# Optimization experiments

Measured on AMD Instinct MI355X. Metric: run time of the kernel, lower is better.

Reference implementation:

```python
import jax, jax.numpy as jnp
import numpy as np

B, S, IN, OUT, E, K = 4, 4096, 1024, 1024, 8, 2
SCALE = 512.0  # alpha / r = 512 / 1
TEMP = 1.0


def setup_inputs() -> dict:
    key = jax.random.key(0)
    k1, k2, k3, k4 = jax.random.split(key, 4)
    return {
        "x": jax.random.normal(k1, (B, S, IN), dtype=jnp.float32),
        "lora_A": jax.random.normal(k2, (E, 1, IN), dtype=jnp.float32) * 0.02,
        "lora_B": jax.random.normal(k3, (E, OUT, 1), dtype=jnp.float32) * 0.02,
        "gate_w": jax.random.normal(k4, (E, IN), dtype=jnp.float32) * 0.02,
        "gate_b": jnp.zeros((E,), dtype=jnp.float32),
    }


def reference(x, lora_A, lora_B, gate_w, gate_b):
    # segment-level gating: mean over seq, softmax over experts
    seg = x.mean(axis=1)                                    # [B, IN]
    logits = (seg @ gate_w.T + gate_b) / TEMP               # [B, E]
    gate_scores = jax.nn.softmax(logits, axis=-1)           # [B, E]
    topk_scores, topk_idx = jax.lax.top_k(gate_scores, K)   # [B, K] (same for all tokens in segment)

    # dense all-expert LoRA compute (eval mode: dropout is identity)
    h = jnp.einsum('bsi,eri->bser', x, lora_A)              # [B, S, E, r]
    expert_outputs = jnp.einsum('bser,eor->bseo', h, lora_B) * SCALE  # [B, S, E, OUT]

    # gather top-k experts per segment (broadcast over seq) and weighted-sum
    sel = jnp.take_along_axis(expert_outputs, topk_idx[:, None, :, None], axis=2)  # [B, S, K, OUT]
    out = jnp.sum(sel * topk_scores[:, None, :, None], axis=2)  # [B, S, OUT]
    return out
```

## Files before the change

kernel.cpp:

```cpp
#include <hip/hip_runtime.h>

#define SCALE_F 512.0f

#define WS_H     0
#define WS_GPART 131072
#define WS_SELC  147456

__global__ __launch_bounds__(256) void k1_h_gate(
    const float* __restrict__ x, const float* __restrict__ lora_A,
    const float* __restrict__ gate_w, float* __restrict__ h,
    float* __restrict__ gpart)
{
    const int tid  = threadIdx.x;
    const int w    = tid >> 6;
    const int lane = tid & 63;
    const int tok0 = blockIdx.x * 8;

    __shared__ float xbuf[8 * 1024];

    float4 W[4][4];
#pragma unroll
    for (int rr = 0; rr < 4; ++rr) {
        const int row = 4 * w + rr;
        const float* rp = (row < 8) ? (lora_A + row * 1024)
                                    : (gate_w + (row - 8) * 1024);
        const float4* rp4 = (const float4*)rp;
#pragma unroll
        for (int j = 0; j < 4; ++j) W[rr][j] = rp4[lane + 64 * j];
    }

    const float4* src = (const float4*)(x + (size_t)tok0 * 1024);
    float4* dst = (float4*)xbuf;
#pragma unroll
    for (int j = 0; j < 8; ++j) dst[tid + 256 * j] = src[tid + 256 * j];
    __syncthreads();

    float gacc0 = 0.f, gacc1 = 0.f, gacc2 = 0.f, gacc3 = 0.f;

#pragma unroll 2
    for (int t = 0; t < 8; ++t) {
        const float4* xr = (const float4*)(xbuf + t * 1024);
        const float4 xv0 = xr[lane];
        const float4 xv1 = xr[lane + 64];
        const float4 xv2 = xr[lane + 128];
        const float4 xv3 = xr[lane + 192];

        float p[4];
#pragma unroll
        for (int rr = 0; rr < 4; ++rr) {
            const float4 a0 = W[rr][0], a1 = W[rr][1];
            const float4 a2 = W[rr][2], a3 = W[rr][3];
            float s;
            s  = xv0.x * a0.x + xv0.y * a0.y + xv0.z * a0.z + xv0.w * a0.w;
            s += xv1.x * a1.x + xv1.y * a1.y + xv1.z * a1.z + xv1.w * a1.w;
            s += xv2.x * a2.x + xv2.y * a2.y + xv2.z * a2.z + xv2.w * a2.w;
            s += xv3.x * a3.x + xv3.y * a3.y + xv3.z * a3.z + xv3.w * a3.w;
            p[rr] = s;
        }
#pragma unroll
        for (int off = 32; off > 0; off >>= 1) {
            p[0] += __shfl_xor(p[0], off);
            p[1] += __shfl_xor(p[1], off);
            p[2] += __shfl_xor(p[2], off);
            p[3] += __shfl_xor(p[3], off);
        }
        const int tok = tok0 + t;
        if (w < 2) {
            if (lane == 0) {
                float4 hv = make_float4(p[0], p[1], p[2], p[3]);
                *(float4*)(h + (size_t)tok * 8 + w * 4) = hv;
            }
        } else {
            gacc0 += p[0]; gacc1 += p[1]; gacc2 += p[2]; gacc3 += p[3];
        }
    }

    if (w >= 2 && lane == 0) {
        float4 gv = make_float4(gacc0, gacc1, gacc2, gacc3);
        *(float4*)(gpart + (size_t)blockIdx.x * 8 + (w - 2) * 4) = gv;
    }
}

__global__ __launch_bounds__(256) void k2_gate(
    const float* __restrict__ gpart, const float* __restrict__ gate_b,
    int* __restrict__ sel, float* __restrict__ coef)
{
    const int tid  = threadIdx.x;
    const int j    = tid & 7;
    const int pair = tid >> 3;
    const int b    = pair >> 3;
    const int e    = pair & 7;

    __shared__ float s_red[32][8];
    __shared__ float s_logit[32];

    float acc = 0.f;
#pragma unroll 8
    for (int k = 0; k < 64; ++k) {
        acc += gpart[(size_t)(b * 512 + j * 64 + k) * 8 + e];
    }
    s_red[pair][j] = acc;
    __syncthreads();

    if (j == 0) {
        float s = 0.f;
#pragma unroll
        for (int q = 0; q < 8; ++q) s += s_red[pair][q];
        s_logit[pair] = s * (1.0f / 4096.0f) + gate_b[e];
    }
    __syncthreads();

    if (tid < 4) {
        float sc[8];
        float m = -1e30f;
#pragma unroll
        for (int q = 0; q < 8; ++q) { sc[q] = s_logit[tid * 8 + q]; m = fmaxf(m, sc[q]); }
        float sum = 0.f;
#pragma unroll
        for (int q = 0; q < 8; ++q) { sc[q] = __expf(sc[q] - m); sum += sc[q]; }
        const float inv = 1.0f / sum;

        int i0 = 0;
#pragma unroll
        for (int q = 1; q < 8; ++q) if (sc[q] > sc[i0]) i0 = q;
        int i1 = (i0 == 0) ? 1 : 0;
#pragma unroll
        for (int q = 0; q < 8; ++q) if (q != i0 && sc[q] > sc[i1]) i1 = q;

        sel[tid * 2]      = i0;
        sel[tid * 2 + 1]  = i1;
        coef[tid * 2]     = SCALE_F * sc[i0] * inv;
        coef[tid * 2 + 1] = SCALE_F * sc[i1] * inv;
    }
}

__global__ __launch_bounds__(256) void k3_combine(
    const float* __restrict__ h, const int* __restrict__ sel,
    const float* __restrict__ coef, const float* __restrict__ lora_B,
    float* __restrict__ out)
{
    const int tid = threadIdx.x;
    const int blk = blockIdx.x;
    const int b   = blk >> 9;

    const int   i0 = sel[b * 2];
    const int   i1 = sel[b * 2 + 1];
    const float c0 = coef[b * 2];
    const float c1 = coef[b * 2 + 1];

    const float4 b0 = ((const float4*)(lora_B + i0 * 1024))[tid];
    const float4 b1 = ((const float4*)(lora_B + i1 * 1024))[tid];
    const float4 v0 = make_float4(c0 * b0.x, c0 * b0.y, c0 * b0.z, c0 * b0.w);
    const float4 v1 = make_float4(c1 * b1.x, c1 * b1.y, c1 * b1.z, c1 * b1.w);

    const int tok0 = blk * 8;
    float4* out4 = (float4*)out;
#pragma unroll
    for (int t = 0; t < 8; ++t) {
        const int tok = tok0 + t;
        const float h0 = h[tok * 8 + i0];
        const float h1 = h[tok * 8 + i1];
        float4 r;
        r.x = h0 * v0.x + h1 * v1.x;
        r.y = h0 * v0.y + h1 * v1.y;
        r.z = h0 * v0.z + h1 * v1.z;
        r.w = h0 * v0.w + h1 * v1.w;
        out4[(size_t)tok * 256 + tid] = r;
    }
}

extern "C" void kernel_launch(void* const* d_in, const int* in_sizes, int n_in,
                              void* d_out, int out_size, void* d_ws, size_t ws_size,
                              hipStream_t stream) {
    const float* x      = (const float*)d_in[0];
    const float* lora_A = (const float*)d_in[1];
    const float* lora_B = (const float*)d_in[2];
    const float* gate_w = (const float*)d_in[3];
    const float* gate_b = (const float*)d_in[4];
    float* out = (float*)d_out;

    float* ws    = (float*)d_ws;
    float* h     = ws + WS_H;
    float* gpart = ws + WS_GPART;
    int*   sel   = (int*)(ws + WS_SELC);
    float* coef  = ws + WS_SELC + 8;

    k1_h_gate<<<2048, 256, 0, stream>>>(x, lora_A, gate_w, h, gpart);
    k2_gate<<<1, 256, 0, stream>>>(gpart, gate_b, sel, coef);
    k3_combine<<<2048, 256, 0, stream>>>(h, sel, coef, lora_B, out);
}
```

Before: 136.8 us.

## Fuse gate softmax/top-k into combine kernel and defer gate shuffle reduction

Drops the single-block gate kernel: every combine block now reduces the 512 per-block gate partials for its batch, then does its own softmax and top-k before writing output. In the first kernel, the gate-row warps accumulate per-lane partials across tokens and do one cross-lane shuffle reduction at the end instead of one per token, and h is staged in shared memory for the combine step. This removes a launch and a serialized tiny kernel, but each of 2048 blocks redundantly reads 16KB of partials plus several syncs.

```diff
diff --git a/kernel.cpp b/kernel.cpp
--- a/kernel.cpp
+++ b/kernel.cpp
@@ -4,9 +4,8 @@
 
 #define WS_H     0
 #define WS_GPART 131072
-#define WS_SELC  147456
-
-__global__ __launch_bounds__(256) void k1_h_gate(
+
+__global__ __launch_bounds__(256) void kA_h_gate(
     const float* __restrict__ x, const float* __restrict__ lora_A,
     const float* __restrict__ gate_w, float* __restrict__ h,
     float* __restrict__ gpart)
@@ -35,7 +34,7 @@
     for (int j = 0; j < 8; ++j) dst[tid + 256 * j] = src[tid + 256 * j];
     __syncthreads();
 
-    float gacc0 = 0.f, gacc1 = 0.f, gacc2 = 0.f, gacc3 = 0.f;
+    float gacc[4] = {0.f, 0.f, 0.f, 0.f};
 
 #pragma unroll 2
     for (int t = 0; t < 8; ++t) {
@@ -57,68 +56,102 @@
             s += xv3.x * a3.x + xv3.y * a3.y + xv3.z * a3.z + xv3.w * a3.w;
             p[rr] = s;
         }
-#pragma unroll
-        for (int off = 32; off > 0; off >>= 1) {
-            p[0] += __shfl_xor(p[0], off);
-            p[1] += __shfl_xor(p[1], off);
-            p[2] += __shfl_xor(p[2], off);
-            p[3] += __shfl_xor(p[3], off);
-        }
-        const int tok = tok0 + t;
+
         if (w < 2) {
+#pragma unroll
+            for (int off = 32; off > 0; off >>= 1) {
+                p[0] += __shfl_xor(p[0], off);
+                p[1] += __shfl_xor(p[1], off);
+                p[2] += __shfl_xor(p[2], off);
+                p[3] += __shfl_xor(p[3], off);
+            }
             if (lane == 0) {
                 float4 hv = make_float4(p[0], p[1], p[2], p[3]);
-                *(float4*)(h + (size_t)tok * 8 + w * 4) = hv;
+                *(float4*)(h + (size_t)(tok0 + t) * 8 + w * 4) = hv;
             }
         } else {
-            gacc0 += p[0]; gacc1 += p[1]; gacc2 += p[2]; gacc3 += p[3];
-        }
-    }
-
-    if (w >= 2 && lane == 0) {
-        float4 gv = make_float4(gacc0, gacc1, gacc2, gacc3);
-        *(float4*)(gpart + (size_t)blockIdx.x * 8 + (w - 2) * 4) = gv;
-    }
-}
-
-__global__ __launch_bounds__(256) void k2_gate(
-    const float* __restrict__ gpart, const float* __restrict__ gate_b,
-    int* __restrict__ sel, float* __restrict__ coef)
+            gacc[0] += p[0]; gacc[1] += p[1]; gacc[2] += p[2]; gacc[3] += p[3];
+        }
+    }
+
+    if (w >= 2) {
+#pragma unroll
+        for (int off = 32; off > 0; off >>= 1) {
+            gacc[0] += __shfl_xor(gacc[0], off);
+            gacc[1] += __shfl_xor(gacc[1], off);
+            gacc[2] += __shfl_xor(gacc[2], off);
+            gacc[3] += __shfl_xor(gacc[3], off);
+        }
+        if (lane == 0) {
+            float4 gv = make_float4(gacc[0], gacc[1], gacc[2], gacc[3]);
+            *(float4*)(gpart + (size_t)blockIdx.x * 8 + (w - 2) * 4) = gv;
+        }
+    }
+}
+
+static __device__ __forceinline__ float4 f4add(float4 a, float4 b) {
+    return make_float4(a.x + b.x, a.y + b.y, a.z + b.z, a.w + b.w);
+}
+
+__global__ __launch_bounds__(256) void kB_gate_combine(
+    const float* __restrict__ h, const float* __restrict__ gpart,
+    const float* __restrict__ gate_b, const float* __restrict__ lora_B,
+    float* __restrict__ out)
 {
     const int tid  = threadIdx.x;
-    const int j    = tid & 7;
-    const int pair = tid >> 3;
-    const int b    = pair >> 3;
-    const int e    = pair & 7;
-
-    __shared__ float s_red[32][8];
-    __shared__ float s_logit[32];
-
-    float acc = 0.f;
-#pragma unroll 8
-    for (int k = 0; k < 64; ++k) {
-        acc += gpart[(size_t)(b * 512 + j * 64 + k) * 8 + e];
-    }
-    s_red[pair][j] = acc;
-    __syncthreads();
-
-    if (j == 0) {
-        float s = 0.f;
-#pragma unroll
-        for (int q = 0; q < 8; ++q) s += s_red[pair][q];
-        s_logit[pair] = s * (1.0f / 4096.0f) + gate_b[e];
-    }
-    __syncthreads();
-
-    if (tid < 4) {
+    const int blk  = blockIdx.x;
+    const int b    = blk >> 9;
+    const int tok0 = blk * 8;
+
+    __shared__ float4 s4[256];
+    __shared__ float  s_h[64];
+    __shared__ float  s_logit[8];
+    __shared__ int    s_sel[2];
+    __shared__ float  s_coef[2];
+
+    const float4* gp4 = (const float4*)(gpart + (size_t)b * 4096);
+    float4 acc = gp4[tid];
+    acc = f4add(acc, gp4[tid + 256]);
+    acc = f4add(acc, gp4[tid + 512]);
+    acc = f4add(acc, gp4[tid + 768]);
+    s4[tid] = acc;
+
+    if (tid < 64) s_h[tid] = h[(size_t)tok0 * 8 + tid];
+    __syncthreads();
+
+    if (tid < 64) {
+        float4 a = f4add(f4add(s4[tid], s4[tid + 64]),
+                         f4add(s4[tid + 128], s4[tid + 192]));
+        s4[tid] = a;
+    }
+    __syncthreads();
+    if (tid < 16) {
+        float4 a = f4add(f4add(s4[tid], s4[tid + 16]),
+                         f4add(s4[tid + 32], s4[tid + 48]));
+        s4[tid] = a;
+    }
+    __syncthreads();
+    if (tid < 2) {
+        float4 a = s4[tid];
+#pragma unroll
+        for (int q = 2; q < 16; q += 2) a = f4add(a, s4[tid + q]);
+        const float inv = 1.0f / 4096.0f;
+        s_logit[tid * 4 + 0] = a.x * inv + gate_b[tid * 4 + 0];
+        s_logit[tid * 4 + 1] = a.y * inv + gate_b[tid * 4 + 1];
+        s_logit[tid * 4 + 2] = a.z * inv + gate_b[tid * 4 + 2];
+        s_logit[tid * 4 + 3] = a.w * inv + gate_b[tid * 4 + 3];
+    }
+    __syncthreads();
+
+    if (tid == 0) {
         float sc[8];
         float m = -1e30f;
 #pragma unroll
-        for (int q = 0; q < 8; ++q) { sc[q] = s_logit[tid * 8 + q]; m = fmaxf(m, sc[q]); }
+        for (int q = 0; q < 8; ++q) { sc[q] = s_logit[q]; m = fmaxf(m, sc[q]); }
         float sum = 0.f;
 #pragma unroll
         for (int q = 0; q < 8; ++q) { sc[q] = __expf(sc[q] - m); sum += sc[q]; }
-        const float inv = 1.0f / sum;
+        const float invs = 1.0f / sum;
 
         int i0 = 0;
 #pragma unroll
@@ -127,45 +160,34 @@
 #pragma unroll
         for (int q = 0; q < 8; ++q) if (q != i0 && sc[q] > sc[i1]) i1 = q;
 
-        sel[tid * 2]      = i0;
-        sel[tid * 2 + 1]  = i1;
-        coef[tid * 2]     = SCALE_F * sc[i0] * inv;
-        coef[tid * 2 + 1] = SCALE_F * sc[i1] * inv;
-    }
-}
-
-__global__ __launch_bounds__(256) void k3_combine(
-    const float* __restrict__ h, const int* __restrict__ sel,
-    const float* __restrict__ coef, const float* __restrict__ lora_B,
-    float* __restrict__ out)
-{
-    const int tid = threadIdx.x;
-    const int blk = blockIdx.x;
-    const int b   = blk >> 9;
-
-    const int   i0 = sel[b * 2];
-    const int   i1 = sel[b * 2 + 1];
-    const float c0 = coef[b * 2];
-    const float c1 = coef[b * 2 + 1];
+        s_sel[0]  = i0;
+        s_sel[1]  = i1;
+        s_coef[0] = SCALE_F * sc[i0] * invs;
+        s_coef[1] = SCALE_F * sc[i1] * invs;
+    }
+    __syncthreads();
+
+    const int   i0 = s_sel[0];
+    const int   i1 = s_sel[1];
+    const float c0 = s_coef[0];
+    const float c1 = s_coef[1];
 
     const float4 b0 = ((const float4*)(lora_B + i0 * 1024))[tid];
     const float4 b1 = ((const float4*)(lora_B + i1 * 1024))[tid];
     const float4 v0 = make_float4(c0 * b0.x, c0 * b0.y, c0 * b0.z, c0 * b0.w);
     const float4 v1 = make_float4(c1 * b1.x, c1 * b1.y, c1 * b1.z, c1 * b1.w);
 
-    const int tok0 = blk * 8;
     float4* out4 = (float4*)out;
 #pragma unroll
     for (int t = 0; t < 8; ++t) {
-        const int tok = tok0 + t;
-        const float h0 = h[tok * 8 + i0];
-        const float h1 = h[tok * 8 + i1];
+        const float h0 = s_h[t * 8 + i0];
+        const float h1 = s_h[t * 8 + i1];
         float4 r;
         r.x = h0 * v0.x + h1 * v1.x;
         r.y = h0 * v0.y + h1 * v1.y;
         r.z = h0 * v0.z + h1 * v1.z;
         r.w = h0 * v0.w + h1 * v1.w;
-        out4[(size_t)tok * 256 + tid] = r;
+        out4[(size_t)(tok0 + t) * 256 + tid] = r;
     }
 }
 
@@ -182,10 +204,7 @@
     float* ws    = (float*)d_ws;
     float* h     = ws + WS_H;
     float* gpart = ws + WS_GPART;
-    int*   sel   = (int*)(ws + WS_SELC);
-    float* coef  = ws + WS_SELC + 8;
-
-    k1_h_gate<<<2048, 256, 0, stream>>>(x, lora_A, gate_w, h, gpart);
-    k2_gate<<<1, 256, 0, stream>>>(gpart, gate_b, sel, coef);
-    k3_combine<<<2048, 256, 0, stream>>>(h, sel, coef, lora_B, out);
-}
+
+    kA_h_gate<<<2048, 256, 0, stream>>>(x, lora_A, gate_w, h, gpart);
+    kB_gate_combine<<<2048, 256, 0, stream>>>(h, gpart, gate_b, lora_B, out);
+}
```

Result: faster. 128.7 us (-5.9%).
